# Kernel tuning notes

Hardware: AMD Instinct MI355X
Metric: run time of the kernel (lower is better)

## Reference

```python
import jax, jax.numpy as jnp
import numpy as np

B, N, C, H = 2, 2048, 1024, 16
D = C // H  # head_dim = 64


def setup_inputs() -> dict:
    key = jax.random.key(0)
    k1, k2, k3, k4 = jax.random.split(key, 4)
    x = jax.random.normal(k1, (B, N, C), dtype=jnp.float32)
    # params (torch Linear: y = x @ W.T + b). Store as [in, out] for einsum.
    w_qkv = jax.random.normal(k2, (C, 3 * C), dtype=jnp.float32) * (1.0 / np.sqrt(C))
    w_out = jax.random.normal(k3, (C, C), dtype=jnp.float32) * (1.0 / np.sqrt(C))
    b_out = jax.random.normal(k4, (C,), dtype=jnp.float32) * 0.01
    # causal mask: 1 above the diagonal -> masked_fill(-inf)
    attn_mask = jnp.triu(jnp.ones((N, N), dtype=jnp.int32), k=1)
    return {"x": x, "w_qkv": w_qkv, "w_out": w_out, "b_out": b_out, "attn_mask": attn_mask}


def reference(x, w_qkv, w_out, b_out, attn_mask):
    b, n, c = x.shape
    scale = 1.0 / jnp.sqrt(jnp.asarray(D, dtype=x.dtype))
    qkv = jnp.einsum('bnc,cd->bnd', x, w_qkv)                # [B, N, 3C]
    qkv = qkv.reshape(b, n, 3, H, D)
    q = qkv[:, :, 0].transpose(0, 2, 1, 3)                   # [B, H, N, D]
    k = qkv[:, :, 1].transpose(0, 2, 1, 3)
    v = qkv[:, :, 2].transpose(0, 2, 1, 3)
    scores = jnp.einsum('bhqd,bhkd->bhqk', q, k) * scale     # [B, H, N, N]
    scores = jnp.where(attn_mask == 1, jnp.asarray(-jnp.inf, dtype=scores.dtype), scores)
    attn = jax.nn.softmax(scores, axis=-1)
    # dropout is identity in eval mode (deterministic reference)
    out = jnp.einsum('bhqk,bhkd->bhqd', attn, v)             # [B, H, N, D]
    out = out.transpose(0, 2, 1, 3).reshape(b, n, c)         # [B, N, C]
    return jnp.einsum('bnc,cd->bnd', out, w_out) + b_out
```

## Files before the change

kernel.cpp:

```cpp
#include <hip/hip_runtime.h>

typedef _Float16 f16;
typedef _Float16 f16x8 __attribute__((ext_vector_type(8)));
typedef _Float16 f16x4 __attribute__((ext_vector_type(4)));
typedef float    f32x4 __attribute__((ext_vector_type(4)));

#define MFMA16(a, b, c) __builtin_amdgcn_mfma_f32_16x16x32_f16((a), (b), (c), 0, 0, 0)

__device__ __forceinline__ void gload16(const void* g, void* l) {
  __builtin_amdgcn_global_load_lds(
      (const __attribute__((address_space(1))) unsigned int*)g,
      (__attribute__((address_space(3))) unsigned int*)l, 16, 0, 0);
}

__device__ __forceinline__ float ex2(float x) {
  float r;
  asm("v_exp_f32 %0, %1" : "=v"(r) : "v"(x));
  return r;
}


__global__ void cast_f32_f16(const float* __restrict__ in, f16* __restrict__ out, int n4) {
  int i = blockIdx.x * blockDim.x + threadIdx.x;
  if (i < n4) {
    float4 v = ((const float4*)in)[i];
    f16x4 o;
    o.x = (f16)v.x; o.y = (f16)v.y; o.z = (f16)v.z; o.w = (f16)v.w;
    ((f16x4*)out)[i] = o;
  }
}

__global__ void transpose_cast(const float* __restrict__ in, f16* __restrict__ out, int R, int Cc) {
  __shared__ float tile[32][33];
  int c0 = blockIdx.x * 32, r0 = blockIdx.y * 32;
  int tx = threadIdx.x, ty = threadIdx.y;
#pragma unroll
  for (int i = ty; i < 32; i += 8)
    tile[i][tx] = in[(size_t)(r0 + i) * Cc + c0 + tx];
  __syncthreads();
#pragma unroll
  for (int i = ty; i < 32; i += 8)
    out[(size_t)(c0 + i) * R + r0 + tx] = (f16)tile[tx][i];
}

template <int KDIM>
__device__ __forceinline__ void gemm_core(const f16* __restrict__ A, const f16* __restrict__ Bt,
                                          int bm, int bn, f16* lA, f16* lB, f32x4 acc[4][4]) {
  const int t = threadIdx.x, lane = t & 63, wave = t >> 6;
  const int wm = wave >> 1, wn = wave & 1;
  const int srow = lane >> 3;
  const int skb = (lane & 7) * 16;
  const int nkt = KDIM / 64;
  for (int kt = 0; kt < nkt; ++kt) {
    __syncthreads();
#pragma unroll
    for (int c = 0; c < 4; ++c) {
      int cc = c * 4 + wave;
      int row = cc * 8 + srow;
      int kbs = skb ^ ((row & 7) << 4);
      gload16((const char*)A + (size_t)(bm * 128 + row) * (KDIM * 2) + kt * 128 + kbs,
              lA + cc * 512);
      gload16((const char*)Bt + (size_t)(bn * 128 + row) * (KDIM * 2) + kt * 128 + kbs,
              lB + cc * 512);
    }
    __syncthreads();
#pragma unroll
    for (int ks = 0; ks < 2; ++ks) {
      f16x8 af[4], bf[4];
#pragma unroll
      for (int mi = 0; mi < 4; ++mi) {
        int r = wm * 64 + mi * 16 + (lane & 15);
        int ke = (ks * 32 + ((lane >> 4) << 3)) ^ ((r & 7) << 3);
        af[mi] = *(const f16x8*)&lA[r * 64 + ke];
      }
#pragma unroll
      for (int ni = 0; ni < 4; ++ni) {
        int r = wn * 64 + ni * 16 + (lane & 15);
        int ke = (ks * 32 + ((lane >> 4) << 3)) ^ ((r & 7) << 3);
        bf[ni] = *(const f16x8*)&lB[r * 64 + ke];
      }
#pragma unroll
      for (int mi = 0; mi < 4; ++mi)
#pragma unroll
        for (int ni = 0; ni < 4; ++ni)
          acc[mi][ni] = MFMA16(af[mi], bf[ni], acc[mi][ni]);
    }
  }
}

__global__ __launch_bounds__(256, 2) void gemm_qkv(const f16* __restrict__ A,
                                                   const f16* __restrict__ Bt,
                                                   f16* __restrict__ Qo, f16* __restrict__ Ko,
                                                   f16* __restrict__ Vt) {
  __shared__ __align__(16) f16 lA[128 * 64];
  __shared__ __align__(16) f16 lB[128 * 64];
  f32x4 acc[4][4] = {};
  int w = blockIdx.x;
  int xcd = w & 7, i = w >> 3;
  int xr = xcd >> 1, xc = xcd & 1;
  int bm = xr * 8 + (i & 7);
  int bn = xc * 12 + (i >> 3);
  gemm_core<1024>(A, Bt, bm, bn, lA, lB, acc);
  int lane = threadIdx.x & 63, wave = threadIdx.x >> 6;
  int wm = wave >> 1, wn = wave & 1;
  int sec = (bn * 128) >> 10;
  float scl = (sec == 0) ? 0.18033688f : 1.0f;
#pragma unroll
  for (int mi = 0; mi < 4; ++mi)
#pragma unroll
    for (int ni = 0; ni < 4; ++ni)
#pragma unroll
      for (int reg = 0; reg < 4; ++reg) {
        int gr = bm * 128 + wm * 64 + mi * 16 + ((lane >> 4) << 2) + reg;
        int gc = bn * 128 + wn * 64 + ni * 16 + (lane & 15);
        int b = gr >> 11, n = gr & 2047;
        int jj = gc & 1023;
        int h = jj >> 6, d = jj & 63;
        f16 v = (f16)(acc[mi][ni][reg] * scl);
        size_t bh = (size_t)(b * 16 + h);
        if (sec == 0)      Qo[(bh * 2048 + n) * 64 + d] = v;
        else if (sec == 1) Ko[(bh * 2048 + n) * 64 + d] = v;
        else {
          int np = (n & ~31) | (((n >> 2) & 3) << 3) | (((n >> 4) & 1) << 2) | (n & 3);
          Vt[(bh * 64 + d) * 2048 + np] = v;
        }
      }
}

__device__ __forceinline__ void attn_one(const f16* __restrict__ Qb, const f16* __restrict__ Kb,
                                         const f16* __restrict__ Vb, f16* __restrict__ Ob,
                                         int qt, int lane, int wave, f16* lK, f16* lV) {
  const int N = 2048;
  const int wq0 = qt * 64 + wave * 16;
  const int g = lane >> 4, q15 = lane & 15;
  f16x8 qf[2];
#pragma unroll
  for (int ks = 0; ks < 2; ++ks)
    qf[ks] = *(const f16x8*)&Qb[(size_t)(wq0 + q15) * 64 + ks * 32 + (g << 3)];
  f32x4 oacc[4] = {};
  float mrun = -1e30f, lrun = 0.f;
  const int srow = lane >> 3, skb = (lane & 7) * 16;
  const int ntiles = qt + 1;

  auto STAGE = [&](int buf, int kv) {
    int kv0 = kv << 6;
#pragma unroll
    for (int c = 0; c < 2; ++c) {
      int cc = c * 4 + wave;
      int row = cc * 8 + srow;
      int kbs = skb ^ ((row & 7) << 4);
      gload16((const char*)Kb + (size_t)(kv0 + row) * 128 + kbs, lK + buf * 4096 + cc * 512);
      gload16((const char*)Vb + (size_t)row * (N * 2) + (size_t)kv0 * 2 + kbs,
              lV + buf * 4096 + cc * 512);
    }
  };

  STAGE(0, 0);
  __syncthreads();
  for (int kv = 0; kv < ntiles; ++kv) {
    int cur = kv & 1;
    if (kv + 1 < ntiles) STAGE(cur ^ 1, kv + 1);
    const f16* K0 = lK + cur * 4096;
    const f16* V0 = lV + cur * 4096;
    int kv0 = kv << 6;
    f32x4 s[4] = {};
    __builtin_amdgcn_s_setprio(1);
#pragma unroll
    for (int ks = 0; ks < 2; ++ks) {
      f16x8 kf[4];
#pragma unroll
      for (int ni = 0; ni < 4; ++ni) {
        int r = ni * 16 + q15;
        int ke = (ks * 32 + (g << 3)) ^ ((r & 7) << 3);
        kf[ni] = *(const f16x8*)&K0[r * 64 + ke];
      }
#pragma unroll
      for (int ni = 0; ni < 4; ++ni) s[ni] = MFMA16(kf[ni], qf[ks], s[ni]);
    }
    __builtin_amdgcn_s_setprio(0);
    if (kv == qt) {
      int gq = wq0 + q15;
#pragma unroll
      for (int ni = 0; ni < 4; ++ni)
#pragma unroll
        for (int reg = 0; reg < 4; ++reg) {
          int gk = kv0 + ni * 16 + g * 4 + reg;
          if (gk > gq) s[ni][reg] = -1e30f;
        }
    }
    f32x4 m4 = s[0];
#pragma unroll
    for (int ni = 1; ni < 4; ++ni)
#pragma unroll
      for (int reg = 0; reg < 4; ++reg) m4[reg] = fmaxf(m4[reg], s[ni][reg]);
    float mx = fmaxf(fmaxf(m4[0], m4[1]), fmaxf(m4[2], m4[3]));
    mx = fmaxf(mx, __shfl_xor(mx, 16));
    mx = fmaxf(mx, __shfl_xor(mx, 32));
    if (__any(mx > mrun)) {
      float mnew = fmaxf(mrun, mx);
      float corr = ex2(mrun - mnew);
      mrun = mnew;
      lrun *= corr;
#pragma unroll
      for (int ni = 0; ni < 4; ++ni)
#pragma unroll
        for (int reg = 0; reg < 4; ++reg) oacc[ni][reg] *= corr;
    }
    float rsum = 0.f;
#pragma unroll
    for (int ni = 0; ni < 4; ++ni)
#pragma unroll
      for (int reg = 0; reg < 4; ++reg) {
        float p = ex2(s[ni][reg] - mrun);
        s[ni][reg] = p;
        rsum += p;
      }
    rsum += __shfl_xor(rsum, 16);
    rsum += __shfl_xor(rsum, 32);
    lrun += rsum;
    f16x8 pf[2];
#pragma unroll
    for (int ks = 0; ks < 2; ++ks)
#pragma unroll
      for (int e = 0; e < 8; ++e) pf[ks][e] = (f16)s[2 * ks + (e >> 2)][e & 3];
    __builtin_amdgcn_s_setprio(1);
#pragma unroll
    for (int ks = 0; ks < 2; ++ks) {
      f16x8 vf[4];
#pragma unroll
      for (int mi = 0; mi < 4; ++mi) {
        int r = mi * 16 + q15;
        int ke = (ks * 32 + (g << 3)) ^ ((r & 7) << 3);
        vf[mi] = *(const f16x8*)&V0[r * 64 + ke];
      }
#pragma unroll
      for (int mi = 0; mi < 4; ++mi) oacc[mi] = MFMA16(vf[mi], pf[ks], oacc[mi]);
    }
    __builtin_amdgcn_s_setprio(0);
    __syncthreads();
  }
  float inv = 1.0f / lrun;
  int gq = wq0 + q15;
#pragma unroll
  for (int mi = 0; mi < 4; ++mi) {
    f16x4 o4;
#pragma unroll
    for (int reg = 0; reg < 4; ++reg) o4[reg] = (f16)(oacc[mi][reg] * inv);
    *(f16x4*)&Ob[(size_t)gq * 1024 + mi * 16 + g * 4] = o4;
  }
}

__global__ __launch_bounds__(256, 2) void attn(const f16* __restrict__ Q,
                                               const f16* __restrict__ K,
                                               const f16* __restrict__ Vt,
                                               f16* __restrict__ O) {
  __shared__ __align__(16) f16 lK[2 * 4096];
  __shared__ __align__(16) f16 lV[2 * 4096];
  int w = blockIdx.x;
  int c = w & 7, j = w >> 3;
  int bh = c * 4 + (j >> 4);
  int x = j & 15;
  int b = bh >> 4, h = bh & 15;
  int lane = threadIdx.x & 63, wave = threadIdx.x >> 6;
  const f16* Qb = Q + (size_t)bh * 2048 * 64;
  const f16* Kb = K + (size_t)bh * 2048 * 64;
  const f16* Vb = Vt + (size_t)bh * 2048 * 64;
  f16* Ob = O + (size_t)b * 2048 * 1024 + h * 64;
  attn_one(Qb, Kb, Vb, Ob, 31 - x, lane, wave, lK, lV);
  attn_one(Qb, Kb, Vb, Ob, x, lane, wave, lK, lV);
}

__global__ __launch_bounds__(256, 2) void gemm_out(const f16* __restrict__ A,
                                                   const f16* __restrict__ Bt,
                                                   const float* __restrict__ bias,
                                                   float* __restrict__ out) {
  __shared__ __align__(16) f16 lA[128 * 64];
  __shared__ __align__(16) f16 lB[128 * 64];
  f32x4 acc[4][4] = {};
  int w = blockIdx.x;
  int xcd = w & 7, i = w >> 3;
  int bm = xcd * 4 + (i & 3);
  int bn = i >> 2;
  gemm_core<1024>(A, Bt, bm, bn, lA, lB, acc);
  int lane = threadIdx.x & 63, wave = threadIdx.x >> 6;
  int wm = wave >> 1, wn = wave & 1;
#pragma unroll
  for (int mi = 0; mi < 4; ++mi)
#pragma unroll
    for (int ni = 0; ni < 4; ++ni)
#pragma unroll
      for (int reg = 0; reg < 4; ++reg) {
        int gr = bm * 128 + wm * 64 + mi * 16 + ((lane >> 4) << 2) + reg;
        int gc = bn * 128 + wn * 64 + ni * 16 + (lane & 15);
        out[(size_t)gr * 1024 + gc] = acc[mi][ni][reg] + bias[gc];
      }
}

extern "C" void kernel_launch(void* const* d_in, const int* in_sizes, int n_in,
                              void* d_out, int out_size, void* d_ws, size_t ws_size,
                              hipStream_t stream) {
  const float* x     = (const float*)d_in[0];
  const float* w_qkv = (const float*)d_in[1];
  const float* w_out = (const float*)d_in[2];
  const float* b_out = (const float*)d_in[3];
  float* out = (float*)d_out;
  char* ws = (char*)d_ws;

  f16* xh    = (f16*)(ws);
  f16* wqkvT = (f16*)(ws + (8u << 20));
  f16* woutT = (f16*)(ws + (14u << 20));
  f16* Qs    = (f16*)(ws + (16u << 20));
  f16* Ks    = (f16*)(ws + (24u << 20));
  f16* Vts   = (f16*)(ws + (32u << 20));
  f16* Oa    = (f16*)(ws + (40u << 20));

  cast_f32_f16<<<4096, 256, 0, stream>>>(x, xh, 1048576);
  transpose_cast<<<dim3(96, 32), dim3(32, 8), 0, stream>>>(w_qkv, wqkvT, 1024, 3072);
  transpose_cast<<<dim3(32, 32), dim3(32, 8), 0, stream>>>(w_out, woutT, 1024, 1024);
  gemm_qkv<<<768, 256, 0, stream>>>(xh, wqkvT, Qs, Ks, Vts);
  attn<<<512, 256, 0, stream>>>(Qs, Ks, Vts, Oa);
  gemm_out<<<256, 256, 0, stream>>>(Oa, woutT, b_out, out);
}
```

Measured before the change: 118.2 us.

## Stage V transpose via LDS, deepen attention prefetch, and split attention blocks

The QKV GEMM epilogue now writes the V section through shared memory, so the permuted transpose goes out as contiguous 16-byte stores instead of scattered scalar writes. The attention kernel prefetches two KV tiles ahead using explicit vmcnt waits and raw barriers in place of __syncthreads. It also launches one query tile per block (1024 blocks, launch bounds raised to 4) instead of pairing a long and a short tile per block, with work ordered longest-first. The row-sum reduction is rewritten as a vector tree add. Risks include load imbalance from the causal work split, register pressure from the higher occupancy bound, and fragile manual waitcnt counting.

```diff
diff --git a/kernel.cpp b/kernel.cpp
--- a/kernel.cpp
+++ b/kernel.cpp
@@ -18,6 +18,10 @@
   asm("v_exp_f32 %0, %1" : "=v"(r) : "v"(x));
   return r;
 }
+
+#define WAITV(N) asm volatile("s_waitcnt vmcnt(" #N ")" ::: "memory")
+#define BARRIER() __builtin_amdgcn_s_barrier()
+#define CFENCE() asm volatile("" ::: "memory")
 
 
 __global__ void cast_f32_f16(const float* __restrict__ in, f16* __restrict__ out, int n4) {
@@ -92,8 +96,9 @@
                                                    const f16* __restrict__ Bt,
                                                    f16* __restrict__ Qo, f16* __restrict__ Ko,
                                                    f16* __restrict__ Vt) {
-  __shared__ __align__(16) f16 lA[128 * 64];
-  __shared__ __align__(16) f16 lB[128 * 64];
+  __shared__ __align__(16) f16 smem[128 * 136];
+  f16* lA = smem;
+  f16* lB = smem + 8192;
   f32x4 acc[4][4] = {};
   int w = blockIdx.x;
   int xcd = w & 7, i = w >> 3;
@@ -103,28 +108,53 @@
   gemm_core<1024>(A, Bt, bm, bn, lA, lB, acc);
   int lane = threadIdx.x & 63, wave = threadIdx.x >> 6;
   int wm = wave >> 1, wn = wave & 1;
+  int g = lane >> 4, q15 = lane & 15;
   int sec = (bn * 128) >> 10;
-  float scl = (sec == 0) ? 0.18033688f : 1.0f;
-#pragma unroll
-  for (int mi = 0; mi < 4; ++mi)
-#pragma unroll
-    for (int ni = 0; ni < 4; ++ni)
-#pragma unroll
-      for (int reg = 0; reg < 4; ++reg) {
-        int gr = bm * 128 + wm * 64 + mi * 16 + ((lane >> 4) << 2) + reg;
-        int gc = bn * 128 + wn * 64 + ni * 16 + (lane & 15);
-        int b = gr >> 11, n = gr & 2047;
-        int jj = gc & 1023;
-        int h = jj >> 6, d = jj & 63;
-        f16 v = (f16)(acc[mi][ni][reg] * scl);
-        size_t bh = (size_t)(b * 16 + h);
-        if (sec == 0)      Qo[(bh * 2048 + n) * 64 + d] = v;
-        else if (sec == 1) Ko[(bh * 2048 + n) * 64 + d] = v;
-        else {
-          int np = (n & ~31) | (((n >> 2) & 3) << 3) | (((n >> 4) & 1) << 2) | (n & 3);
-          Vt[(bh * 64 + d) * 2048 + np] = v;
+  if (sec < 2) {
+    float scl = (sec == 0) ? 0.18033688f : 1.0f;
+#pragma unroll
+    for (int mi = 0; mi < 4; ++mi)
+#pragma unroll
+      for (int ni = 0; ni < 4; ++ni)
+#pragma unroll
+        for (int reg = 0; reg < 4; ++reg) {
+          int gr = bm * 128 + wm * 64 + mi * 16 + (g << 2) + reg;
+          int gc = bn * 128 + wn * 64 + ni * 16 + q15;
+          int b = gr >> 11, n = gr & 2047;
+          int jj = gc & 1023;
+          int h = jj >> 6, d = jj & 63;
+          f16 v = (f16)(acc[mi][ni][reg] * scl);
+          size_t bh = (size_t)(b * 16 + h);
+          if (sec == 0) Qo[(bh * 2048 + n) * 64 + d] = v;
+          else          Ko[(bh * 2048 + n) * 64 + d] = v;
         }
-      }
+  } else {
+    __syncthreads();
+#pragma unroll
+    for (int mi = 0; mi < 4; ++mi)
+#pragma unroll
+      for (int ni = 0; ni < 4; ++ni)
+#pragma unroll
+        for (int reg = 0; reg < 4; ++reg) {
+          int rl = wm * 64 + mi * 16 + (g << 2) + reg;
+          int cl = wn * 64 + ni * 16 + q15;
+          int r5 = rl & 31;
+          int rlp = (rl & ~31) | (((r5 >> 2) & 3) << 3) | (((r5 >> 4) & 1) << 2) | (r5 & 3);
+          smem[cl * 136 + rlp] = (f16)acc[mi][ni][reg];
+        }
+    __syncthreads();
+    int tid = threadIdx.x;
+    int cl = tid >> 1, half = tid & 1;
+    int jj = (bn * 128 + cl) & 1023;
+    int h = jj >> 6, d = jj & 63;
+    int b = (bm * 128) >> 11;
+    size_t bh = (size_t)(b * 16 + h);
+    f16* dst = Vt + (bh * 64 + d) * 2048 + (bm * 128 & 2047) + half * 64;
+    const f16* src = smem + cl * 136 + half * 64;
+#pragma unroll
+    for (int j8 = 0; j8 < 8; ++j8)
+      *(f16x8*)&dst[j8 * 8] = *(const f16x8*)&src[j8 * 8];
+  }
 }
 
 __device__ __forceinline__ void attn_one(const f16* __restrict__ Qb, const f16* __restrict__ Kb,
@@ -156,10 +186,11 @@
   };
 
   STAGE(0, 0);
-  __syncthreads();
+  if (ntiles > 1) STAGE(1, 1);
   for (int kv = 0; kv < ntiles; ++kv) {
     int cur = kv & 1;
-    if (kv + 1 < ntiles) STAGE(cur ^ 1, kv + 1);
+    if (kv + 1 < ntiles) WAITV(4); else WAITV(0);
+    BARRIER();
     const f16* K0 = lK + cur * 4096;
     const f16* V0 = lV + cur * 4096;
     int kv0 = kv << 6;
@@ -206,15 +237,12 @@
 #pragma unroll
         for (int reg = 0; reg < 4; ++reg) oacc[ni][reg] *= corr;
     }
-    float rsum = 0.f;
 #pragma unroll
     for (int ni = 0; ni < 4; ++ni)
 #pragma unroll
-      for (int reg = 0; reg < 4; ++reg) {
-        float p = ex2(s[ni][reg] - mrun);
-        s[ni][reg] = p;
-        rsum += p;
-      }
+      for (int reg = 0; reg < 4; ++reg) s[ni][reg] = ex2(s[ni][reg] - mrun);
+    f32x4 racc = (s[0] + s[1]) + (s[2] + s[3]);
+    float rsum = (racc[0] + racc[1]) + (racc[2] + racc[3]);
     rsum += __shfl_xor(rsum, 16);
     rsum += __shfl_xor(rsum, 32);
     lrun += rsum;
@@ -237,7 +265,9 @@
       for (int mi = 0; mi < 4; ++mi) oacc[mi] = MFMA16(vf[mi], pf[ks], oacc[mi]);
     }
     __builtin_amdgcn_s_setprio(0);
-    __syncthreads();
+    BARRIER();
+    CFENCE();
+    if (kv + 2 < ntiles) STAGE(cur, kv + 2);
   }
   float inv = 1.0f / lrun;
   int gq = wq0 + q15;
@@ -250,7 +280,7 @@
   }
 }
 
-__global__ __launch_bounds__(256, 2) void attn(const f16* __restrict__ Q,
+__global__ __launch_bounds__(256, 4) void attn(const f16* __restrict__ Q,
                                                const f16* __restrict__ K,
                                                const f16* __restrict__ Vt,
                                                f16* __restrict__ O) {
@@ -258,16 +288,15 @@
   __shared__ __align__(16) f16 lV[2 * 4096];
   int w = blockIdx.x;
   int c = w & 7, j = w >> 3;
-  int bh = c * 4 + (j >> 4);
-  int x = j & 15;
+  int bh = c * 4 + (j & 3);
+  int qt = 31 - (j >> 2);
   int b = bh >> 4, h = bh & 15;
   int lane = threadIdx.x & 63, wave = threadIdx.x >> 6;
   const f16* Qb = Q + (size_t)bh * 2048 * 64;
   const f16* Kb = K + (size_t)bh * 2048 * 64;
   const f16* Vb = Vt + (size_t)bh * 2048 * 64;
   f16* Ob = O + (size_t)b * 2048 * 1024 + h * 64;
-  attn_one(Qb, Kb, Vb, Ob, 31 - x, lane, wave, lK, lV);
-  attn_one(Qb, Kb, Vb, Ob, x, lane, wave, lK, lV);
+  attn_one(Qb, Kb, Vb, Ob, qt, lane, wave, lK, lV);
 }
 
 __global__ __launch_bounds__(256, 2) void gemm_out(const f16* __restrict__ A,
@@ -318,6 +347,6 @@
   transpose_cast<<<dim3(96, 32), dim3(32, 8), 0, stream>>>(w_qkv, wqkvT, 1024, 3072);
   transpose_cast<<<dim3(32, 32), dim3(32, 8), 0, stream>>>(w_out, woutT, 1024, 1024);
   gemm_qkv<<<768, 256, 0, stream>>>(xh, wqkvT, Qs, Ks, Vts);
-  attn<<<512, 256, 0, stream>>>(Qs, Ks, Vts, Oa);
+  attn<<<1024, 256, 0, stream>>>(Qs, Ks, Vts, Oa);
   gemm_out<<<256, 256, 0, stream>>>(Oa, woutT, b_out, out);
 }
```

Measured after the change: 106.4 us. 1.11x faster.
